# Optimization experiments

Hardware: AMD Instinct MI355X
Metric: run time of the kernel (lower is better)

The kernel has to match this reference:

```python
import jax, jax.numpy as jnp
import numpy as np

N_NODES = 50000
N_EDGES = 800000
IN_FEATS = 256
HIDDEN = 128
HEADS = 2
NEG_SLOPE = 0.2


def gat_conv(x, edge_index, W, att_src, att_dst, bias, heads, out_c, concat):
    """PyG-style GATConv: linear -> per-edge attention logits -> segment
    softmax over destination neighborhoods -> scatter-add aggregate.
    Self-loops are added (PyG default add_self_loops=True)."""
    N = x.shape[0]
    h = (x @ W.T).reshape(N, heads, out_c)           # [N,H,C]
    loop = jnp.arange(N)
    src = jnp.concatenate([edge_index[0], loop])      # [E+N]
    dst = jnp.concatenate([edge_index[1], loop])
    a_src = jnp.sum(h * att_src, axis=-1)             # [N,H]
    a_dst = jnp.sum(h * att_dst, axis=-1)
    alpha = a_src[src] + a_dst[dst]                   # [E+N,H]
    alpha = jax.nn.leaky_relu(alpha, NEG_SLOPE)
    amax = jax.ops.segment_max(alpha, dst, num_segments=N)
    alpha = jnp.exp(alpha - amax[dst])
    denom = jax.ops.segment_sum(alpha, dst, num_segments=N)
    alpha = alpha / denom[dst]
    msg = h[src] * alpha[..., None]                   # [E+N,H,C]
    out = jax.ops.segment_sum(msg, dst, num_segments=N)  # [N,H,C]
    if concat:
        out = out.reshape(N, heads * out_c)
    else:
        out = out.mean(axis=1)
    return out + bias


def setup_inputs() -> dict:
    key = jax.random.key(0)
    ks = jax.random.split(key, 12)
    x = jax.random.normal(ks[0], (N_NODES, IN_FEATS), dtype=jnp.float32)
    edge_index = jax.random.randint(ks[1], (2, N_EDGES), 0, N_NODES, dtype=jnp.int64)
    s = 0.1
    W1 = jax.random.normal(ks[2], (HEADS * HIDDEN, IN_FEATS), dtype=jnp.float32) * s
    att_src1 = jax.random.normal(ks[3], (1, HEADS, HIDDEN), dtype=jnp.float32) * s
    att_dst1 = jax.random.normal(ks[4], (1, HEADS, HIDDEN), dtype=jnp.float32) * s
    b1 = jnp.zeros((HEADS * HIDDEN,), dtype=jnp.float32)
    W2 = jax.random.normal(ks[5], (HIDDEN, HEADS * HIDDEN), dtype=jnp.float32) * s
    att_src2 = jax.random.normal(ks[6], (1, 1, HIDDEN), dtype=jnp.float32) * s
    att_dst2 = jax.random.normal(ks[7], (1, 1, HIDDEN), dtype=jnp.float32) * s
    b2 = jnp.zeros((HIDDEN,), dtype=jnp.float32)
    return {"x": x, "edge_index": edge_index,
            "W1": W1, "att_src1": att_src1, "att_dst1": att_dst1, "b1": b1,
            "W2": W2, "att_src2": att_src2, "att_dst2": att_dst2, "b2": b2}


def reference(x, edge_index, W1, att_src1, att_dst1, b1, W2, att_src2, att_dst2, b2):
    h = gat_conv(x, edge_index, W1, att_src1, att_dst1, b1, HEADS, HIDDEN, True)
    h = jax.nn.relu(h)
    out = gat_conv(h, edge_index, W2, att_src2, att_dst2, b2, 1, HIDDEN, False)
    return out
```

## Files before the change

### kernel.cpp

```cpp
#include <hip/hip_runtime.h>
#include <hip/hip_bf16.h>


typedef _Float16 half8v __attribute__((ext_vector_type(8)));
typedef _Float16 half4v __attribute__((ext_vector_type(4)));
typedef _Float16 half2v __attribute__((ext_vector_type(2)));
typedef float f32x4 __attribute__((ext_vector_type(4)));


template <typename TA, int H, bool SCATTER>
__global__ __launch_bounds__(256) void gemm_att_kernel(
    const TA* __restrict__ A,
    const float* __restrict__ B,
    _Float16* __restrict__ C,
    const float* __restrict__ att_s,
    const float* __restrict__ att_d,
    float* __restrict__ a_s,
    float* __restrict__ a_d,
    int M, int K,
    const int* __restrict__ esrc, const int* __restrict__ edst,
    int* __restrict__ cursor, int* __restrict__ csr_src, int E)
{
    constexpr int BM = 128, BK = 32, LDA = 40;
    constexpr int NCOL = H * 128;
    __shared__ _Float16 Ah[BM * LDA];
    __shared__ _Float16 Bh[BM * LDA];
    __shared__ float red[2][2][64][2];

    const int tid = threadIdx.x;

    if constexpr (SCATTER) {
        const int nq   = (E + 3) >> 2;
        const int nblk = gridDim.x * gridDim.y;
        const int bid  = blockIdx.y * gridDim.x + blockIdx.x;
        for (int q = bid * 256 + tid; q < nq; q += nblk * 256) {
            const int e4 = q * 4;
            if (e4 + 3 < E) {
                const int4 sv = *reinterpret_cast<const int4*>(esrc + e4);
                const int4 dv = *reinterpret_cast<const int4*>(edst + e4);
                csr_src[atomicAdd(&cursor[dv.x], 1)] = sv.x;
                csr_src[atomicAdd(&cursor[dv.y], 1)] = sv.y;
                csr_src[atomicAdd(&cursor[dv.z], 1)] = sv.z;
                csr_src[atomicAdd(&cursor[dv.w], 1)] = sv.w;
            } else {
                for (int k = e4; k < E; ++k)
                    csr_src[atomicAdd(&cursor[edst[k]], 1)] = esrc[k];
            }
        }
    }

    const int m0 = blockIdx.x * BM;
    const int by = blockIdx.y;
    const int n0 = by * 128;
    const int w  = tid >> 6;
    const int l  = tid & 63;
    const int wm = (w >> 1) * 64;
    const int wn = (w & 1) * 64;
    const int lr = l & 15;
    const int lq = l >> 4;

    f32x4 acc[4][4] = {};

    for (int k0 = 0; k0 < K; k0 += BK) {
        if constexpr (__is_same(TA, float)) {
#pragma unroll
            for (int it = 0; it < 4; ++it) {
                const int row = (tid >> 3) + it * 32;
                const int gm  = min(m0 + row, M - 1);
                const int c4  = (tid & 7) * 4;
                float4 v = *reinterpret_cast<const float4*>(A + (long)gm * K + k0 + c4);
                half4v o = { (_Float16)v.x, (_Float16)v.y, (_Float16)v.z, (_Float16)v.w };
                *reinterpret_cast<half4v*>(&Ah[row * LDA + c4]) = o;
            }
        } else {
#pragma unroll
            for (int it = 0; it < 2; ++it) {
                const int row = (tid >> 2) + it * 64;
                const int gm  = min(m0 + row, M - 1);
                const int c8  = (tid & 3) * 8;
                float4 v = *reinterpret_cast<const float4*>((const char*)A + ((long)gm * K + k0 + c8) * 2);
                *reinterpret_cast<float4*>(&Ah[row * LDA + c8]) = v;
            }
        }
#pragma unroll
        for (int it = 0; it < 4; ++it) {
            const int row = (tid >> 3) + it * 32;
            const int c4  = (tid & 7) * 4;
            float4 v = *reinterpret_cast<const float4*>(B + (long)(n0 + row) * K + k0 + c4);
            half4v o = { (_Float16)v.x, (_Float16)v.y, (_Float16)v.z, (_Float16)v.w };
            *reinterpret_cast<half4v*>(&Bh[row * LDA + c4]) = o;
        }
        __syncthreads();

        half8v af[4], bf[4];
#pragma unroll
        for (int i = 0; i < 4; ++i)
            af[i] = *reinterpret_cast<const half8v*>(&Ah[(wm + i * 16 + lr) * LDA + lq * 8]);
#pragma unroll
        for (int j = 0; j < 4; ++j)
            bf[j] = *reinterpret_cast<const half8v*>(&Bh[(wn + j * 16 + lr) * LDA + lq * 8]);
#pragma unroll
        for (int i = 0; i < 4; ++i)
#pragma unroll
            for (int j = 0; j < 4; ++j)
                acc[i][j] = __builtin_amdgcn_mfma_f32_16x16x32_f16(af[i], bf[j], acc[i][j], 0, 0, 0);
        __syncthreads();
    }

#pragma unroll
    for (int i = 0; i < 4; ++i) {
        const int gm_base = m0 + wm + i * 16 + lq * 4;
#pragma unroll
        for (int r = 0; r < 4; ++r) {
            const int gm = gm_base + r;
            if (gm < M) {
#pragma unroll
                for (int j = 0; j < 4; ++j)
                    C[(long)gm * NCOL + n0 + wn + j * 16 + lr] = (_Float16)acc[i][j][r];
            }
        }
    }

    float asv[4], adv[4];
#pragma unroll
    for (int j = 0; j < 4; ++j) {
        asv[j] = att_s[n0 + wn + j * 16 + lr];
        adv[j] = att_d[n0 + wn + j * 16 + lr];
    }
    float ps[4][4] = {}, pd[4][4] = {};
#pragma unroll
    for (int i = 0; i < 4; ++i)
#pragma unroll
        for (int j = 0; j < 4; ++j)
#pragma unroll
            for (int r = 0; r < 4; ++r) {
                ps[i][r] += acc[i][j][r] * asv[j];
                pd[i][r] += acc[i][j][r] * adv[j];
            }
#pragma unroll
    for (int o = 1; o < 16; o <<= 1)
#pragma unroll
        for (int i = 0; i < 4; ++i)
#pragma unroll
            for (int r = 0; r < 4; ++r) {
                ps[i][r] += __shfl_xor(ps[i][r], o, 64);
                pd[i][r] += __shfl_xor(pd[i][r], o, 64);
            }
    if (lr == 0) {
#pragma unroll
        for (int i = 0; i < 4; ++i)
#pragma unroll
            for (int r = 0; r < 4; ++r) {
                const int row = i * 16 + lq * 4 + r;
                red[wm >> 6][wn >> 6][row][0] = ps[i][r];
                red[wm >> 6][wn >> 6][row][1] = pd[i][r];
            }
    }
    __syncthreads();
    if (wn == 0) {
        const int row = l;
        const int gm = m0 + wm + row;
        if (gm < M) {
            const int wi = wm >> 6;
            a_s[(long)gm * H + by] = red[wi][0][row][0] + red[wi][1][row][0];
            a_d[(long)gm * H + by] = red[wi][0][row][1] + red[wi][1][row][1];
        }
    }
}


__global__ void count_kernel(const int* __restrict__ dst, int* __restrict__ deg, int E)
{
    const int tid = blockIdx.x * blockDim.x + threadIdx.x;
    const int e4 = tid * 4;
    if (e4 + 3 < E) {
        const int4 d = *reinterpret_cast<const int4*>(dst + e4);
        atomicAdd(&deg[d.x], 1);
        atomicAdd(&deg[d.y], 1);
        atomicAdd(&deg[d.z], 1);
        atomicAdd(&deg[d.w], 1);
    } else if (e4 < E) {
        for (int k = e4; k < E; ++k) atomicAdd(&deg[dst[k]], 1);
    }
}

__global__ __launch_bounds__(256) void block_scan_kernel(
    const int* __restrict__ deg, int* __restrict__ pre, int* __restrict__ blk, int n)
{
    __shared__ int s[256];
    const int t = threadIdx.x;
    const int base = blockIdx.x * 1024 + t * 4;
    int4 d = make_int4(-1, -1, -1, -1);
    if (base + 3 < n) d = *reinterpret_cast<const int4*>(deg + base);
    else {
        if (base + 0 < n) d.x = deg[base + 0];
        if (base + 1 < n) d.y = deg[base + 1];
        if (base + 2 < n) d.z = deg[base + 2];
        if (base + 3 < n) d.w = deg[base + 3];
    }
    const int v0 = d.x + 1, v1 = d.y + 1, v2 = d.z + 1, v3 = d.w + 1;
    s[t] = v0 + v1 + v2 + v3;
    __syncthreads();
#pragma unroll
    for (int o = 1; o < 256; o <<= 1) {
        int val = 0;
        if (t >= o) val = s[t - o];
        __syncthreads();
        s[t] += val;
        __syncthreads();
    }
    int run = (t == 0) ? 0 : s[t - 1];
    int4 o4;
    o4.x = run; run += v0;
    o4.y = run; run += v1;
    o4.z = run; run += v2;
    o4.w = run; run += v3;
    if (base + 3 < n) *reinterpret_cast<int4*>(pre + base) = o4;
    else {
        if (base + 0 < n) pre[base + 0] = o4.x;
        if (base + 1 < n) pre[base + 1] = o4.y;
        if (base + 2 < n) pre[base + 2] = o4.z;
        if (base + 3 < n) pre[base + 3] = o4.w;
    }
    if (t == 255) blk[blockIdx.x] = s[255];
}

__global__ __launch_bounds__(256) void finalize_scan_kernel(
    const int* __restrict__ pre, const int* __restrict__ blk,
    int* __restrict__ off, int* __restrict__ cursor, int* __restrict__ csr_src,
    int n, int nvb)
{
    __shared__ int s_add;
    const int vb = blockIdx.x;
    const int t  = threadIdx.x;
    if (t < 64) {
        int v = (t < vb) ? blk[t] : 0;
#pragma unroll
        for (int o = 32; o > 0; o >>= 1) v += __shfl_xor(v, o, 64);
        if (t == 0) s_add = v;
    }
    __syncthreads();
    const int add = s_add;
    const int base = vb * 1024 + t * 4;
    if (base + 3 < n) {
        int4 p = *reinterpret_cast<const int4*>(pre + base);
        p.x += add; p.y += add; p.z += add; p.w += add;
        *reinterpret_cast<int4*>(off + base) = p;
        int4 c = make_int4(p.x + 1, p.y + 1, p.z + 1, p.w + 1);
        *reinterpret_cast<int4*>(cursor + base) = c;
        csr_src[p.x] = base + 0;
        csr_src[p.y] = base + 1;
        csr_src[p.z] = base + 2;
        csr_src[p.w] = base + 3;
    } else {
#pragma unroll
        for (int k = 0; k < 4; ++k)
            if (base + k < n) {
                const int v = pre[base + k] + add;
                off[base + k] = v;
                cursor[base + k] = v + 1;
                csr_src[v] = base + k;
            }
    }
    if (vb == nvb - 1 && t == 0) off[n] = add + blk[vb];
}


#define AGG_TILE 64

template <int H, int C, int VPT, bool RELU, typename TOUT>
__global__ __launch_bounds__(H * C / VPT) void aggregate_kernel(
    const int* __restrict__ csr_off,
    const int* __restrict__ csr_src,
    const _Float16* __restrict__ h,
    const float* __restrict__ a_s,
    const float* __restrict__ a_d,
    const float* __restrict__ bias,
    TOUT* __restrict__ out)
{
    const int d   = blockIdx.x;
    const int t   = threadIdx.x;
    const int col = t * VPT;
    const int hh  = col / C;

    __shared__ int   s_src[AGG_TILE];
    __shared__ float s_w[AGG_TILE][H];

    const int beg = csr_off[d];
    const int end = csr_off[d + 1];

    float acc[VPT] = {};
    float wsum = 0.f;

    for (int base = beg; base < end; base += AGG_TILE) {
        const int len = min(AGG_TILE, end - base);
        if (t < len) {
            const int s = csr_src[base + t];
            s_src[t] = s;
#pragma unroll
            for (int h2 = 0; h2 < H; ++h2) {
                float logit = a_s[s * H + h2] + a_d[d * H + h2];
                logit = logit > 0.f ? logit : 0.2f * logit;
                s_w[t][h2] = __expf(logit);
            }
        }
        __syncthreads();
#pragma unroll 4
        for (int j = 0; j < len; ++j) {
            const float w = s_w[j][hh];
            const int   s = s_src[j];
            if constexpr (VPT == 4) {
                half4v hv = *reinterpret_cast<const half4v*>(h + (long)s * (H * C) + col);
                acc[0] += w * (float)hv.x;
                acc[1] += w * (float)hv.y;
                acc[2] += w * (float)hv.z;
                acc[3] += w * (float)hv.w;
            } else {
                half2v hv = *reinterpret_cast<const half2v*>(h + (long)s * (H * C) + col);
                acc[0] += w * (float)hv.x;
                acc[1] += w * (float)hv.y;
            }
            wsum += w;
        }
        __syncthreads();
    }

    const float inv = 1.f / wsum;
    float r[VPT];
#pragma unroll
    for (int k = 0; k < VPT; ++k) {
        r[k] = acc[k] * inv + bias[col + k];
        if (RELU) r[k] = r[k] > 0.f ? r[k] : 0.f;
    }
    if constexpr (__is_same(TOUT, _Float16)) {
#pragma unroll
        for (int k = 0; k < VPT; ++k)
            out[(long)d * (H * C) + col + k] = (_Float16)r[k];
    } else {
#pragma unroll
        for (int k = 0; k < VPT; ++k)
            out[(long)d * (H * C) + col + k] = r[k];
    }
}


extern "C" void kernel_launch(void* const* d_in, const int* in_sizes, int n_in,
                              void* d_out, int out_size, void* d_ws, size_t ws_size,
                              hipStream_t stream)
{
    const float* x    = (const float*)d_in[0];
    const int*   eidx = (const int*)d_in[1];
    const float* W1   = (const float*)d_in[2];
    const float* as1  = (const float*)d_in[3];
    const float* ad1  = (const float*)d_in[4];
    const float* b1   = (const float*)d_in[5];
    const float* W2   = (const float*)d_in[6];
    const float* as2  = (const float*)d_in[7];
    const float* ad2  = (const float*)d_in[8];
    const float* b2   = (const float*)d_in[9];
    float* out = (float*)d_out;

    const int IN_FEATS = 256;
    const int N = in_sizes[0] / IN_FEATS;
    const int E = in_sizes[1] / 2;

    const int* esrc = eidx;
    const int* edst = eidx + E;

    size_t off = 0;
    auto alloc = [&](size_t bytes) -> void* {
        void* p = (char*)d_ws + off;
        off += (bytes + 255) & ~(size_t)255;
        return p;
    };
    _Float16* h1h   = (_Float16*)alloc((size_t)N * 256 * 2);
    _Float16* o1h   = (_Float16*)alloc((size_t)N * 256 * 2);
    _Float16* h2h   = (_Float16*)alloc((size_t)N * 128 * 2);
    float* a1s      = (float*)alloc((size_t)N * 2 * 4);
    float* a1d      = (float*)alloc((size_t)N * 2 * 4);
    float* a2s      = (float*)alloc((size_t)N * 4);
    float* a2d      = (float*)alloc((size_t)N * 4);
    int*   deg      = (int*)alloc((size_t)N * 4);
    int*   pre      = (int*)alloc((size_t)N * 4);
    int*   cursor   = (int*)alloc((size_t)N * 4);
    int*   csr_off  = (int*)alloc((size_t)(N + 1) * 4);
    int*   csr_src  = (int*)alloc((size_t)(E + N) * 4);
    int*   blk      = (int*)alloc(64 * 4);

    const int nvb = (N + 1023) / 1024;

    hipMemsetAsync(deg, 0, (size_t)N * 4, stream);
    count_kernel<<<((E + 3) / 4 + 255) / 256, 256, 0, stream>>>(edst, deg, E);
    block_scan_kernel<<<nvb, 256, 0, stream>>>(deg, pre, blk, N);
    finalize_scan_kernel<<<nvb, 256, 0, stream>>>(pre, blk, csr_off, cursor, csr_src, N, nvb);

    {
        dim3 grid((N + 127) / 128, 2);
        gemm_att_kernel<float, 2, true><<<grid, 256, 0, stream>>>(
            x, W1, h1h, as1, ad1, a1s, a1d, N, 256,
            esrc, edst, cursor, csr_src, E);
    }
    aggregate_kernel<2, 128, 4, true, _Float16><<<N, 64, 0, stream>>>(
        csr_off, csr_src, h1h, a1s, a1d, b1, o1h);

    {
        dim3 grid((N + 127) / 128, 1);
        gemm_att_kernel<_Float16, 1, false><<<grid, 256, 0, stream>>>(
            o1h, W2, h2h, as2, ad2, a2s, a2d, N, 256,
            nullptr, nullptr, nullptr, nullptr, 0);
    }
    aggregate_kernel<1, 128, 2, false, float><<<N, 64, 0, stream>>>(
        csr_off, csr_src, h2h, a2s, a2d, b2, out);
}
```

Measured before the change: 323.7 us.

## Record per-edge rank in count pass; scatter CSR via dedicated blocks without atomics

The count kernel now saves the atomicAdd return value as each edge's rank within its destination. The CSR fill then writes directly to csr_off[dst]+1+rank with no atomics, dropping the cursor array. Instead of every GEMM block doing scatter work before its tile, 192 extra blocks appended to a 1D grid do the scatter and exit, so the GEMM blocks run unburdened. The cost is an extra E-sized rank buffer that is written once and read back once.

```diff
diff --git a/kernel.cpp b/kernel.cpp
--- a/kernel.cpp
+++ b/kernel.cpp
@@ -17,9 +17,10 @@
     const float* __restrict__ att_d,
     float* __restrict__ a_s,
     float* __restrict__ a_d,
-    int M, int K,
+    int M, int K, int GB,
     const int* __restrict__ esrc, const int* __restrict__ edst,
-    int* __restrict__ cursor, int* __restrict__ csr_src, int E)
+    const int* __restrict__ rank, const int* __restrict__ csr_off,
+    int* __restrict__ csr_src, int E, int nScatBlk)
 {
     constexpr int BM = 128, BK = 32, LDA = 40;
     constexpr int NCOL = H * 128;
@@ -28,29 +29,33 @@
     __shared__ float red[2][2][64][2];
 
     const int tid = threadIdx.x;
+    const int bid = blockIdx.x;
 
     if constexpr (SCATTER) {
-        const int nq   = (E + 3) >> 2;
-        const int nblk = gridDim.x * gridDim.y;
-        const int bid  = blockIdx.y * gridDim.x + blockIdx.x;
-        for (int q = bid * 256 + tid; q < nq; q += nblk * 256) {
-            const int e4 = q * 4;
-            if (e4 + 3 < E) {
-                const int4 sv = *reinterpret_cast<const int4*>(esrc + e4);
-                const int4 dv = *reinterpret_cast<const int4*>(edst + e4);
-                csr_src[atomicAdd(&cursor[dv.x], 1)] = sv.x;
-                csr_src[atomicAdd(&cursor[dv.y], 1)] = sv.y;
-                csr_src[atomicAdd(&cursor[dv.z], 1)] = sv.z;
-                csr_src[atomicAdd(&cursor[dv.w], 1)] = sv.w;
-            } else {
-                for (int k = e4; k < E; ++k)
-                    csr_src[atomicAdd(&cursor[edst[k]], 1)] = esrc[k];
-            }
-        }
-    }
-
-    const int m0 = blockIdx.x * BM;
-    const int by = blockIdx.y;
+        if (bid >= GB * H) {
+            const int sbid = bid - GB * H;
+            const int nq = (E + 3) >> 2;
+            for (int q = sbid * 256 + tid; q < nq; q += nScatBlk * 256) {
+                const int e4 = q * 4;
+                if (e4 + 3 < E) {
+                    const int4 sv = *reinterpret_cast<const int4*>(esrc + e4);
+                    const int4 dv = *reinterpret_cast<const int4*>(edst + e4);
+                    const int4 rv = *reinterpret_cast<const int4*>(rank + e4);
+                    csr_src[csr_off[dv.x] + 1 + rv.x] = sv.x;
+                    csr_src[csr_off[dv.y] + 1 + rv.y] = sv.y;
+                    csr_src[csr_off[dv.z] + 1 + rv.z] = sv.z;
+                    csr_src[csr_off[dv.w] + 1 + rv.w] = sv.w;
+                } else {
+                    for (int k = e4; k < E; ++k)
+                        csr_src[csr_off[edst[k]] + 1 + rank[k]] = esrc[k];
+                }
+            }
+            return;
+        }
+    }
+
+    const int m0 = (bid % GB) * BM;
+    const int by = bid / GB;
     const int n0 = by * 128;
     const int w  = tid >> 6;
     const int l  = tid & 63;
@@ -169,18 +174,21 @@
 }
 
 
-__global__ void count_kernel(const int* __restrict__ dst, int* __restrict__ deg, int E)
+__global__ void count_kernel(const int* __restrict__ dst, int* __restrict__ deg,
+                             int* __restrict__ rank, int E)
 {
     const int tid = blockIdx.x * blockDim.x + threadIdx.x;
     const int e4 = tid * 4;
     if (e4 + 3 < E) {
         const int4 d = *reinterpret_cast<const int4*>(dst + e4);
-        atomicAdd(&deg[d.x], 1);
-        atomicAdd(&deg[d.y], 1);
-        atomicAdd(&deg[d.z], 1);
-        atomicAdd(&deg[d.w], 1);
+        int4 r;
+        r.x = atomicAdd(&deg[d.x], 1);
+        r.y = atomicAdd(&deg[d.y], 1);
+        r.z = atomicAdd(&deg[d.z], 1);
+        r.w = atomicAdd(&deg[d.w], 1);
+        *reinterpret_cast<int4*>(rank + e4) = r;
     } else if (e4 < E) {
-        for (int k = e4; k < E; ++k) atomicAdd(&deg[dst[k]], 1);
+        for (int k = e4; k < E; ++k) rank[k] = atomicAdd(&deg[dst[k]], 1);
     }
 }
 
@@ -227,8 +235,7 @@
 
 __global__ __launch_bounds__(256) void finalize_scan_kernel(
     const int* __restrict__ pre, const int* __restrict__ blk,
-    int* __restrict__ off, int* __restrict__ cursor, int* __restrict__ csr_src,
-    int n, int nvb)
+    int* __restrict__ off, int* __restrict__ csr_src, int n, int nvb)
 {
     __shared__ int s_add;
     const int vb = blockIdx.x;
@@ -246,8 +253,6 @@
         int4 p = *reinterpret_cast<const int4*>(pre + base);
         p.x += add; p.y += add; p.z += add; p.w += add;
         *reinterpret_cast<int4*>(off + base) = p;
-        int4 c = make_int4(p.x + 1, p.y + 1, p.z + 1, p.w + 1);
-        *reinterpret_cast<int4*>(cursor + base) = c;
         csr_src[p.x] = base + 0;
         csr_src[p.y] = base + 1;
         csr_src[p.z] = base + 2;
@@ -258,7 +263,6 @@
             if (base + k < n) {
                 const int v = pre[base + k] + add;
                 off[base + k] = v;
-                cursor[base + k] = v + 1;
                 csr_src[v] = base + k;
             }
     }
@@ -382,7 +386,7 @@
     float* a2d      = (float*)alloc((size_t)N * 4);
     int*   deg      = (int*)alloc((size_t)N * 4);
     int*   pre      = (int*)alloc((size_t)N * 4);
-    int*   cursor   = (int*)alloc((size_t)N * 4);
+    int*   rank     = (int*)alloc((size_t)E * 4);
     int*   csr_off  = (int*)alloc((size_t)(N + 1) * 4);
     int*   csr_src  = (int*)alloc((size_t)(E + N) * 4);
     int*   blk      = (int*)alloc(64 * 4);
@@ -390,24 +394,25 @@
     const int nvb = (N + 1023) / 1024;
 
     hipMemsetAsync(deg, 0, (size_t)N * 4, stream);
-    count_kernel<<<((E + 3) / 4 + 255) / 256, 256, 0, stream>>>(edst, deg, E);
+    count_kernel<<<((E + 3) / 4 + 255) / 256, 256, 0, stream>>>(edst, deg, rank, E);
     block_scan_kernel<<<nvb, 256, 0, stream>>>(deg, pre, blk, N);
-    finalize_scan_kernel<<<nvb, 256, 0, stream>>>(pre, blk, csr_off, cursor, csr_src, N, nvb);
+    finalize_scan_kernel<<<nvb, 256, 0, stream>>>(pre, blk, csr_off, csr_src, N, nvb);
 
     {
-        dim3 grid((N + 127) / 128, 2);
-        gemm_att_kernel<float, 2, true><<<grid, 256, 0, stream>>>(
-            x, W1, h1h, as1, ad1, a1s, a1d, N, 256,
-            esrc, edst, cursor, csr_src, E);
+        const int GB = (N + 127) / 128;
+        const int nScat = 192;
+        gemm_att_kernel<float, 2, true><<<GB * 2 + nScat, 256, 0, stream>>>(
+            x, W1, h1h, as1, ad1, a1s, a1d, N, 256, GB,
+            esrc, edst, rank, csr_off, csr_src, E, nScat);
     }
     aggregate_kernel<2, 128, 4, true, _Float16><<<N, 64, 0, stream>>>(
         csr_off, csr_src, h1h, a1s, a1d, b1, o1h);
 
     {
-        dim3 grid((N + 127) / 128, 1);
-        gemm_att_kernel<_Float16, 1, false><<<grid, 256, 0, stream>>>(
-            o1h, W2, h2h, as2, ad2, a2s, a2d, N, 256,
-            nullptr, nullptr, nullptr, nullptr, 0);
+        const int GB = (N + 127) / 128;
+        gemm_att_kernel<_Float16, 1, false><<<GB, 256, 0, stream>>>(
+            o1h, W2, h2h, as2, ad2, a2s, a2d, N, 256, GB,
+            nullptr, nullptr, nullptr, nullptr, nullptr, 0, 0);
     }
     aggregate_kernel<1, 128, 2, false, float><<<N, 64, 0, stream>>>(
         csr_off, csr_src, h2h, a2s, a2d, b2, out);
```

Result: faster. 291.2 us (-10.1%).
